# Kernel optimization log

Hardware: AMD Instinct MI355X
Metric: run time of the kernel (lower is better)

## Reference

```python
import jax, jax.numpy as jnp
import numpy as np

N1 = 64
N2 = 64
K = 12        # k_max truncated Fourier modes
L = 4         # num_layers
CIN = 1
COUT = 1
B, H, W = 16, 256, 256


def _conv1x1(x, w, b):
    # x: [B,Ci,H,W], w: [Co,Ci], b: [Co]
    return jnp.einsum('bchw,oc->bohw', x, w) + b[None, :, None, None]


def _spectral_conv(x, w1, w2):
    # x: [B,C,H,W] real; w1,w2: [Ci,Co,K,K] complex64
    Bb, C, Hh, Ww = x.shape
    x_ft = jnp.fft.rfft2(x, axes=(-2, -1))  # [B,C,H,W//2+1] complex
    top = jnp.einsum('bimn,iomn->bomn', x_ft[:, :, :K, :K], w1)
    bot = jnp.einsum('bimn,iomn->bomn', x_ft[:, :, -K:, :K], w2)
    out_ft = jnp.zeros((Bb, N2, Hh, Ww // 2 + 1), dtype=jnp.complex64)
    out_ft = out_ft.at[:, :, :K, :K].set(top)
    out_ft = out_ft.at[:, :, -K:, :K].set(bot)
    return jnp.fft.irfft2(out_ft, s=(Hh, Ww), axes=(-2, -1))


def setup_inputs() -> dict:
    key = jax.random.key(0)
    ks = jax.random.split(key, 12)
    scale = 1.0 / (N1 * N2)
    inp = {
        'x': jax.random.normal(ks[0], (B, CIN, H, W), jnp.float32),
        'lift_w': jax.random.normal(ks[1], (N1, CIN), jnp.float32) * 0.5,
        'lift_b': jnp.zeros((N1,), jnp.float32),
        'spec1_re': jax.random.normal(ks[2], (L, N1, N2, K, K), jnp.float32) * scale,
        'spec1_im': jax.random.normal(ks[3], (L, N1, N2, K, K), jnp.float32) * scale,
        'spec2_re': jax.random.normal(ks[4], (L, N1, N2, K, K), jnp.float32) * scale,
        'spec2_im': jax.random.normal(ks[5], (L, N1, N2, K, K), jnp.float32) * scale,
        'skip_w': jax.random.normal(ks[6], (L, N2, N1), jnp.float32) * (1.0 / np.sqrt(N1)),
        'skip_b': jnp.zeros((L, N2), jnp.float32),
        'proj_w': jax.random.normal(ks[7], (COUT, N2), jnp.float32) * (1.0 / np.sqrt(N2)),
        'proj_b': jnp.zeros((COUT,), jnp.float32),
    }
    return inp


def reference(x, lift_w, lift_b, spec1_re, spec1_im, spec2_re, spec2_im,
              skip_w, skip_b, proj_w, proj_b):
    h = _conv1x1(x, lift_w, lift_b)  # [B,N1,H,W]
    for l in range(L):
        w1 = (spec1_re[l] + 1j * spec1_im[l]).astype(jnp.complex64)
        w2 = (spec2_re[l] + 1j * spec2_im[l]).astype(jnp.complex64)
        spec = _spectral_conv(h, w1, w2)
        skip = _conv1x1(h, skip_w[l], skip_b[l])
        h = jax.nn.gelu(spec + skip, approximate=False)  # torch nn.GELU default = exact erf
    return _conv1x1(h, proj_w, proj_b)  # [B,Cout,H,W]
```

## Files before the change

### kernel.cpp

```cpp
#include <hip/hip_runtime.h>
#include <math.h>

#define PI2 6.283185307179586f

typedef short  bf16x8 __attribute__((ext_vector_type(8)));
typedef float  f32x4  __attribute__((ext_vector_type(4)));
typedef unsigned int u32x4 __attribute__((ext_vector_type(4)));
typedef unsigned int u32x2 __attribute__((ext_vector_type(2)));

__device__ __forceinline__ float gelu_exact(float x) {
    return 0.5f * x * (1.0f + erff(x * 0.70710678118654752f));
}
__device__ __forceinline__ float gelu_fast(float x) {
    float ax = __builtin_fabsf(x);
    float s  = ax * 0.70710678118654752f;
    float t  = 1.0f / fmaf(0.3275911f, s, 1.0f);
    float u  = fmaf(t, 1.061405429f, -1.453152027f);
    u = fmaf(t, u, 1.421413741f);
    u = fmaf(t, u, -0.284496736f);
    u = fmaf(t, u, 0.254829592f);
    float p  = t * u;
    float e  = __expf(-s * s);
    float q  = 0.5f * ax;
    return fmaf(-q * p, e, fmaf(0.5f, x, q));
}
__device__ __forceinline__ float bf2f(unsigned short u) {
    return __uint_as_float(((unsigned int)u) << 16);
}
__device__ __forceinline__ unsigned short f2bf(float f) {
    unsigned int b = __float_as_uint(f);
    unsigned int r = (b + 0x7FFFu + ((b >> 16) & 1u)) >> 16;
    return (unsigned short)r;
}
__device__ __forceinline__ unsigned cvtpk_bf16(float lo, float hi) {
    unsigned r;
    asm("v_cvt_pk_bf16_f32 %0, %1, %2" : "=v"(r) : "v"(lo), "v"(hi));
    return r;
}
__device__ __forceinline__ unsigned pack_lo(unsigned a, unsigned b) {
    return (a & 0xffffu) | (b << 16);
}
__device__ __forceinline__ unsigned pack_hi(unsigned a, unsigned b) {
    return (a >> 16) | (b & 0xffff0000u);
}

template<bool BF> struct HS;
template<> struct HS<false> {
    using ST = float;
    static __device__ __forceinline__ float4 ld4(const ST* p, size_t i4) {
        return reinterpret_cast<const float4*>(p)[i4];
    }
    static __device__ __forceinline__ void st4(ST* p, size_t i4, float4 v) {
        reinterpret_cast<float4*>(p)[i4] = v;
    }
};
template<> struct HS<true> {
    using ST = unsigned short;
    static __device__ __forceinline__ float4 ld4(const ST* p, size_t i4) {
        ushort4 u = reinterpret_cast<const ushort4*>(p)[i4];
        return make_float4(bf2f(u.x), bf2f(u.y), bf2f(u.z), bf2f(u.w));
    }
    static __device__ __forceinline__ void st4(ST* p, size_t i4, float4 v) {
        ushort4 u = make_ushort4(f2bf(v.x), f2bf(v.y), f2bf(v.z), f2bf(v.w));
        reinterpret_cast<ushort4*>(p)[i4] = u;
    }
};


template<bool BF>
__global__ void k_lift(const float* __restrict__ x, const float* __restrict__ lw,
                       const float* __restrict__ lb, typename HS<BF>::ST* __restrict__ h) {
    int i = blockIdx.x * 256 + threadIdx.x;
    int p4 = i & 16383;
    int bc = i >> 14;
    int c = bc & 63, b = bc >> 6;
    float4 xv = reinterpret_cast<const float4*>(x)[(size_t)b * 16384 + p4];
    float w = lw[c], bias = lb[c];
    float4 o;
    o.x = fmaf(xv.x, w, bias); o.y = fmaf(xv.y, w, bias);
    o.z = fmaf(xv.z, w, bias); o.w = fmaf(xv.w, w, bias);
    HS<BF>::st4(h, i, o);
}

template<bool BF>
__global__ __launch_bounds__(256) void k_coldft(const typename HS<BF>::ST* __restrict__ h,
                                                float2* __restrict__ Xw) {
    using ST = typename HS<BF>::ST;
    __shared__ __align__(16) ST xs[64 * 264];
    __shared__ __align__(16) float2 ct[12 * 258];
    int tid = threadIdx.x;
    size_t row0 = (size_t)blockIdx.x * 64;
#pragma unroll
    for (int k = 0; k < 12; k++) {
        int idx = tid + k * 256;
        int n = idx >> 8, w = idx & 255;
        int rr = (n * w) & 255;
        float s, c;
        __sincosf(PI2 * (float)rr * (1.0f / 256.0f), &s, &c);
        ct[n * 258 + w] = make_float2(c, -s);
    }
    const ST* src = h + row0 * 256;
    if constexpr (BF) {
#pragma unroll
        for (int k = 0; k < 8; k++) {
            int i = (tid + k * 256) * 8;
            int r = i >> 8, w = i & 255;
            uint4 v = *reinterpret_cast<const uint4*>(src + i);
            *reinterpret_cast<uint4*>(&xs[r * 264 + w]) = v;
        }
    } else {
#pragma unroll
        for (int k = 0; k < 16; k++) {
            int i = (tid + k * 256) * 4;
            int r = i >> 8, w = i & 255;
            float4 v = *reinterpret_cast<const float4*>(src + i);
            *reinterpret_cast<float4*>(&xs[r * 264 + w]) = v;
        }
    }
    __syncthreads();
    int r = tid >> 2, g = tid & 3;
    int n0 = g * 3;
    float a0r = 0.f, a0i = 0.f, a1r = 0.f, a1i = 0.f, a2r = 0.f, a2i = 0.f;
    const ST* xrow = &xs[r * 264];
    const float2* c0 = &ct[(n0 + 0) * 258];
    const float2* c1 = &ct[(n0 + 1) * 258];
    const float2* c2 = &ct[(n0 + 2) * 258];
#pragma unroll 8
    for (int wc = 0; wc < 256; wc += 4) {
        float x0, x1, x2, x3;
        if constexpr (BF) {
            ushort4 u = *reinterpret_cast<const ushort4*>(xrow + wc);
            x0 = bf2f(u.x); x1 = bf2f(u.y); x2 = bf2f(u.z); x3 = bf2f(u.w);
        } else {
            float4 f = *reinterpret_cast<const float4*>(xrow + wc);
            x0 = f.x; x1 = f.y; x2 = f.z; x3 = f.w;
        }
        float4 pa, pb;
        pa = *reinterpret_cast<const float4*>(c0 + wc);
        pb = *reinterpret_cast<const float4*>(c0 + wc + 2);
        a0r = fmaf(x0, pa.x, a0r); a0i = fmaf(x0, pa.y, a0i);
        a0r = fmaf(x1, pa.z, a0r); a0i = fmaf(x1, pa.w, a0i);
        a0r = fmaf(x2, pb.x, a0r); a0i = fmaf(x2, pb.y, a0i);
        a0r = fmaf(x3, pb.z, a0r); a0i = fmaf(x3, pb.w, a0i);
        pa = *reinterpret_cast<const float4*>(c1 + wc);
        pb = *reinterpret_cast<const float4*>(c1 + wc + 2);
        a1r = fmaf(x0, pa.x, a1r); a1i = fmaf(x0, pa.y, a1i);
        a1r = fmaf(x1, pa.z, a1r); a1i = fmaf(x1, pa.w, a1i);
        a1r = fmaf(x2, pb.x, a1r); a1i = fmaf(x2, pb.y, a1i);
        a1r = fmaf(x3, pb.z, a1r); a1i = fmaf(x3, pb.w, a1i);
        pa = *reinterpret_cast<const float4*>(c2 + wc);
        pb = *reinterpret_cast<const float4*>(c2 + wc + 2);
        a2r = fmaf(x0, pa.x, a2r); a2i = fmaf(x0, pa.y, a2i);
        a2r = fmaf(x1, pa.z, a2r); a2i = fmaf(x1, pa.w, a2i);
        a2r = fmaf(x2, pb.x, a2r); a2i = fmaf(x2, pb.y, a2i);
        a2r = fmaf(x3, pb.z, a2r); a2i = fmaf(x3, pb.w, a2i);
    }
    size_t bc = row0 >> 8;
    int hrow = (int)(row0 & 255) + r;
    float2* dst = Xw + (bc * 12) * 256 + hrow;
    dst[(size_t)(n0 + 0) * 256] = make_float2(a0r, a0i);
    dst[(size_t)(n0 + 1) * 256] = make_float2(a1r, a1i);
    dst[(size_t)(n0 + 2) * 256] = make_float2(a2r, a2i);
}

__global__ void k_rowdft(const float2* __restrict__ Xw, float2* __restrict__ F) {
    __shared__ float2 sm[12 * 257];
    int bc = blockIdx.x;
    const float2* src = Xw + (size_t)bc * 3072;
    for (int idx = threadIdx.x; idx < 3072; idx += 256) {
        int n = idx >> 8, hh = idx & 255;
        sm[n * 257 + hh] = src[idx];
    }
    __syncthreads();
    for (int j = threadIdx.x; j < 288; j += 256) {
        int n = j % 12, mm = j / 12;
        int meff = (mm < 12) ? mm : mm - 24;
        float s, c;
        __sincosf(-PI2 * (float)meff * (1.0f / 256.0f), &s, &c);
        float br = c, bi = s;
        float tr = 1.f, ti = 0.f, Fr = 0.f, Fi = 0.f;
        for (int hh = 0; hh < 256; hh++) {
            float2 xv = sm[n * 257 + hh];
            Fr = fmaf(xv.x, tr, Fr); Fr = fmaf(-xv.y, ti, Fr);
            Fi = fmaf(xv.x, ti, Fi); Fi = fmaf(xv.y, tr, Fi);
            float nr = tr * br - ti * bi;
            ti = tr * bi + ti * br;
            tr = nr;
        }
        F[(size_t)bc * 288 + j] = make_float2(Fr, Fi);
    }
}

__global__ void k_specmul(const float2* __restrict__ F,
                          const float* __restrict__ s1r, const float* __restrict__ s1i,
                          const float* __restrict__ s2r, const float* __restrict__ s2i,
                          float2* __restrict__ Y, int l) {
    __shared__ float2 wsh[4096];
    int mm = blockIdx.x / 12, n = blockIdx.x % 12;
    const float* wr; const float* wi; int m;
    if (mm < 12) { wr = s1r; wi = s1i; m = mm; }
    else         { wr = s2r; wi = s2i; m = mm - 12; }
    size_t base = (size_t)l * 589824 + (size_t)m * 12 + n;
    for (int idx = threadIdx.x; idx < 4096; idx += 256) {
        size_t a = base + (size_t)idx * 144;
        wsh[idx] = make_float2(wr[a], wi[a]);
    }
    __syncthreads();
    int o = threadIdx.x & 63, bq = threadIdx.x >> 6;
    for (int it = 0; it < 4; it++) {
        int b = bq * 4 + it;
        float Yr = 0.f, Yi = 0.f;
        const float2* Fb = F + (size_t)b * 64 * 288 + mm * 12 + n;
        for (int c = 0; c < 64; c++) {
            float2 fc = Fb[(size_t)c * 288];
            float2 wv = wsh[c * 64 + o];
            Yr = fmaf(fc.x, wv.x, Yr); Yr = fmaf(-fc.y, wv.y, Yr);
            Yi = fmaf(fc.x, wv.y, Yi); Yi = fmaf(fc.y, wv.x, Yi);
        }
        Y[((size_t)b * 64 + o) * 288 + mm * 12 + n] = make_float2(Yr, Yi);
    }
}

__global__ void k_expand(const float2* __restrict__ Y, float2* __restrict__ G) {
    int t = blockIdx.x * 256 + threadIdx.x;
    int hh = t & 255;
    int rem = t >> 8;
    int n = rem % 12, bo = rem / 12;
    const float2* Yb = Y + (size_t)bo * 288 + n;
    float s, c;
    __sincosf(PI2 * (float)hh * (1.0f / 256.0f), &s, &c);
    float br = c, bi = s;
    float tr = 1.f, ti = 0.f, Gr = 0.f, Gi = 0.f;
#pragma unroll
    for (int mm = 0; mm < 12; mm++) {
        float2 yv = Yb[mm * 12];
        Gr = fmaf(yv.x, tr, Gr); Gr = fmaf(-yv.y, ti, Gr);
        Gi = fmaf(yv.x, ti, Gi); Gi = fmaf(yv.y, tr, Gi);
        float nr = tr * br - ti * bi;
        ti = tr * bi + ti * br;
        tr = nr;
    }
    ti = -ti;
#pragma unroll
    for (int mm = 12; mm < 24; mm++) {
        float2 yv = Yb[mm * 12];
        Gr = fmaf(yv.x, tr, Gr); Gr = fmaf(-yv.y, ti, Gr);
        Gi = fmaf(yv.x, ti, Gi); Gi = fmaf(yv.y, tr, Gi);
        float nr = tr * br - ti * bi;
        ti = tr * bi + ti * br;
        tr = nr;
    }
    float sc = (n == 0 ? 1.0f : 2.0f) * (1.0f / 65536.0f);
    G[t] = make_float2(Gr * sc, Gi * sc);
}

template<bool BF>
__global__ __launch_bounds__(256) void k_update(
        typename HS<BF>::ST* __restrict__ h, const float2* __restrict__ G,
        const float* __restrict__ skw, const float* __restrict__ skb, int l) {
    __shared__ float hin[64 * 64];
    __shared__ float swT[64 * 68];
    __shared__ float2 Gs[64 * 12];
    __shared__ float2 ctab[12 * 64];
    int bx = blockIdx.x;
    int wt = bx & 3, hrow = (bx >> 2) & 255, b = bx >> 10;
    int w0 = wt * 64;
    int tid = threadIdx.x;
    size_t base4 = (size_t)b * 1048576 + (size_t)hrow * 64 + (w0 >> 2);
#pragma unroll
    for (int k = 0; k < 4; k++) {
        int idx = tid + k * 256;
        int c = idx >> 4, q = idx & 15;
        reinterpret_cast<float4*>(hin)[c * 16 + q] =
            HS<BF>::ld4(h, base4 + (size_t)c * 16384 + q);
    }
#pragma unroll
    for (int k = 0; k < 16; k++) {
        int idx = tid + k * 256;
        swT[(idx & 63) * 68 + (idx >> 6)] = skw[l * 4096 + idx];
    }
#pragma unroll
    for (int k = 0; k < 3; k++) {
        int idx = tid + k * 256;
        int o = idx / 12, n = idx % 12;
        Gs[idx] = G[(((size_t)b * 64 + o) * 12 + n) * 256 + hrow];
    }
#pragma unroll
    for (int k = 0; k < 3; k++) {
        int idx = tid + k * 256;
        int n = idx >> 6, wl = idx & 63;
        int r = (n * (w0 + wl)) & 255;
        float s, c;
        __sincosf(PI2 * (float)r * (1.0f / 256.0f), &s, &c);
        ctab[idx] = make_float2(c, s);
    }
    __syncthreads();
    int wq = tid & 15, oq = tid >> 4;
    float acc[4][4];
#pragma unroll
    for (int jo = 0; jo < 4; jo++) {
        float bias = skb[l * 64 + oq * 4 + jo];
#pragma unroll
        for (int jw = 0; jw < 4; jw++) acc[jo][jw] = bias;
    }
#pragma unroll
    for (int n = 0; n < 12; n++) {
        float2 g0 = Gs[(oq * 4 + 0) * 12 + n];
        float2 g1 = Gs[(oq * 4 + 1) * 12 + n];
        float2 g2 = Gs[(oq * 4 + 2) * 12 + n];
        float2 g3 = Gs[(oq * 4 + 3) * 12 + n];
#pragma unroll
        for (int jw = 0; jw < 4; jw++) {
            float2 cs = ctab[n * 64 + wq * 4 + jw];
            acc[0][jw] = fmaf(g0.x, cs.x, acc[0][jw]); acc[0][jw] = fmaf(-g0.y, cs.y, acc[0][jw]);
            acc[1][jw] = fmaf(g1.x, cs.x, acc[1][jw]); acc[1][jw] = fmaf(-g1.y, cs.y, acc[1][jw]);
            acc[2][jw] = fmaf(g2.x, cs.x, acc[2][jw]); acc[2][jw] = fmaf(-g2.y, cs.y, acc[2][jw]);
            acc[3][jw] = fmaf(g3.x, cs.x, acc[3][jw]); acc[3][jw] = fmaf(-g3.y, cs.y, acc[3][jw]);
        }
    }
    const float4* hin4 = reinterpret_cast<const float4*>(hin);
    const float4* swT4 = reinterpret_cast<const float4*>(swT);
#pragma unroll 4
    for (int c = 0; c < 64; c++) {
        float4 hv = hin4[c * 16 + wq];
        float4 wv = swT4[c * 17 + oq];
        acc[0][0] = fmaf(wv.x, hv.x, acc[0][0]); acc[0][1] = fmaf(wv.x, hv.y, acc[0][1]);
        acc[0][2] = fmaf(wv.x, hv.z, acc[0][2]); acc[0][3] = fmaf(wv.x, hv.w, acc[0][3]);
        acc[1][0] = fmaf(wv.y, hv.x, acc[1][0]); acc[1][1] = fmaf(wv.y, hv.y, acc[1][1]);
        acc[1][2] = fmaf(wv.y, hv.z, acc[1][2]); acc[1][3] = fmaf(wv.y, hv.w, acc[1][3]);
        acc[2][0] = fmaf(wv.z, hv.x, acc[2][0]); acc[2][1] = fmaf(wv.z, hv.y, acc[2][1]);
        acc[2][2] = fmaf(wv.z, hv.z, acc[2][2]); acc[2][3] = fmaf(wv.z, hv.w, acc[2][3]);
        acc[3][0] = fmaf(wv.w, hv.x, acc[3][0]); acc[3][1] = fmaf(wv.w, hv.y, acc[3][1]);
        acc[3][2] = fmaf(wv.w, hv.z, acc[3][2]); acc[3][3] = fmaf(wv.w, hv.w, acc[3][3]);
    }
#pragma unroll
    for (int jo = 0; jo < 4; jo++) {
        int o = oq * 4 + jo;
        float4 r;
        r.x = gelu_exact(acc[jo][0]); r.y = gelu_exact(acc[jo][1]);
        r.z = gelu_exact(acc[jo][2]); r.w = gelu_exact(acc[jo][3]);
        HS<BF>::st4(h, base4 + (size_t)o * 16384 + wq, r);
    }
}

template<bool BF>
__global__ void k_proj(const typename HS<BF>::ST* __restrict__ h, const float* __restrict__ pw,
                       const float* __restrict__ pb, float* __restrict__ out) {
    int i = blockIdx.x * 256 + threadIdx.x;
    int b = i >> 14, p4 = i & 16383;
    size_t hb = (size_t)b * 1048576 + p4;
    float4 acc = make_float4(0.f, 0.f, 0.f, 0.f);
#pragma unroll 8
    for (int c = 0; c < 64; c++) {
        float4 hv = HS<BF>::ld4(h, hb + (size_t)c * 16384);
        float wv = pw[c];
        acc.x = fmaf(hv.x, wv, acc.x); acc.y = fmaf(hv.y, wv, acc.y);
        acc.z = fmaf(hv.z, wv, acc.z); acc.w = fmaf(hv.w, wv, acc.w);
    }
    float bias = pb[0];
    acc.x += bias; acc.y += bias; acc.z += bias; acc.w += bias;
    reinterpret_cast<float4*>(out)[i] = acc;
}

#define SKWHI 22528
#define SKWLO 38912
#define TW2US 55296
__global__ __launch_bounds__(256) void k_ttab(unsigned short* __restrict__ Tg,
                                              const float* __restrict__ skw) {
    int idx = blockIdx.x * 256 + threadIdx.x;
    if (idx >= 79872) return;
    if (idx < 16384) {
        int q = idx & 8191;
        int w = q >> 5, b3 = (q >> 3) & 3;
        int k2 = ((b3 ^ (w & 3)) << 3) | (q & 7);
        float v = 0.f;
        if (k2 < 24) {
            int n = k2 >> 1, r = (n * w) & 255;
            float s, c;
            __sincosf(PI2 * (float)r * (1.0f / 256.0f), &s, &c);
            v = (k2 & 1) ? s : c;
        }
        if (idx < 8192) Tg[idx] = f2bf(v);
        else { unsigned short hi = f2bf(v); Tg[idx] = f2bf(v - bf2f(hi)); }
    } else if (idx < 22528) {
        int q = idx - 16384;
        int n2 = q >> 8, t = q & 255;
        int w = (((t >> 3) ^ (n2 & 7)) << 3) | (t & 7);
        int n = n2 >> 1, r = (n * w) & 255;
        float s, c;
        __sincosf(PI2 * (float)r * (1.0f / 256.0f), &s, &c);
        Tg[idx] = f2bf((n2 & 1) ? s : c);
    } else if (idx < 55296) {
        int q = idx - SKWHI;
        int lo = (q >= 16384);
        q &= 16383;
        float w = skw[q];
        unsigned short hi = f2bf(w);
        Tg[idx] = lo ? f2bf(w - bf2f(hi)) : hi;
    } else {
        int j = idx - TW2US;
        int pair = j >> 1, comp = j & 1;
        int mm = pair >> 8, hh = pair & 255;
        int meff = (mm < 12) ? mm : mm - 24;
        int r = (((-(meff * hh)) % 256) + 256) & 255;
        float s, c;
        __sincosf(PI2 * (float)r * (1.0f / 256.0f), &s, &c);
        reinterpret_cast<float*>(Tg + TW2US)[j] = comp ? s : c;
    }
}

__global__ __launch_bounds__(256) void k_xw0(const float* __restrict__ xg,
                                             const float* __restrict__ lw,
                                             const float* __restrict__ lb,
                                             unsigned short* __restrict__ Xwp) {
    __shared__ float xr[256];
    __shared__ float part[24][9];
    __shared__ float xh[24];
    int blk = blockIdx.x;
    int tid = threadIdx.x;
    if (tid < 64)
        reinterpret_cast<float4*>(xr)[tid] =
            reinterpret_cast<const float4*>(xg + (size_t)blk * 256)[tid];
    __syncthreads();
    if (tid < 192) {
        int n2 = tid % 24, seg = tid / 24;
        int n = n2 >> 1, comp = n2 & 1;
        float acc = 0.f;
#pragma unroll 8
        for (int j = 0; j < 32; j++) {
            int w = seg * 32 + j;
            int r = (n * w) & 255;
            float s, c;
            __sincosf(PI2 * (float)r * (1.0f / 256.0f), &s, &c);
            acc = fmaf(xr[w], comp ? -s : c, acc);
        }
        part[n2][seg] = acc;
    }
    __syncthreads();
    if (tid < 24) {
        float a = 0.f;
#pragma unroll
        for (int s = 0; s < 8; s++) a += part[tid][s];
        xh[tid] = a;
    }
    __syncthreads();
    unsigned* dstw = reinterpret_cast<unsigned*>(Xwp + (size_t)blk * 3072);
#pragma unroll
    for (int q = 0; q < 3; q++) {
        int i = tid + q * 256;
        int c = i / 12, n = i % 12;
        float wr = lw[c];
        float re = fmaf(wr, xh[2 * n], (n == 0) ? lb[c] * 256.0f : 0.0f);
        float im = wr * xh[2 * n + 1];
        unsigned short hre = f2bf(re), him = f2bf(im);
        unsigned short lre = f2bf(re - bf2f(hre)), lim = f2bf(im - bf2f(him));
        dstw[i] = (unsigned)hre | ((unsigned)him << 16);
        dstw[768 + i] = (unsigned)lre | ((unsigned)lim << 16);
    }
}

__global__ __launch_bounds__(256) void k_rowdft2t(const unsigned short* __restrict__ Xwp,
                                                  float2* __restrict__ F,
                                                  const float2* __restrict__ tw2) {
    __shared__ float2 sm[12 * 257];
    int bc = blockIdx.x;
    int b = bc >> 6, c = bc & 63;
    for (int idx = threadIdx.x; idx < 3072; idx += 256) {
        int hh = idx / 12, n = idx % 12;
        size_t base = ((size_t)(b * 256 + hh)) * 3072 + c * 24 + n * 2;
        unsigned hi = *reinterpret_cast<const unsigned*>(Xwp + base);
        unsigned lo = *reinterpret_cast<const unsigned*>(Xwp + base + 1536);
        float re = bf2f((unsigned short)(hi & 0xffff)) + bf2f((unsigned short)(lo & 0xffff));
        float im = bf2f((unsigned short)(hi >> 16)) + bf2f((unsigned short)(lo >> 16));
        sm[n * 257 + hh] = make_float2(re, im);
    }
    __syncthreads();
    for (int j = threadIdx.x; j < 288; j += 256) {
        int n = j % 12, mm = j / 12;
        const float2* twp = tw2 + mm * 256;
        const float2* smp = &sm[n * 257];
        float Fr = 0.f, Fi = 0.f;
#pragma unroll 8
        for (int hh = 0; hh < 256; hh++) {
            float2 xv = smp[hh];
            float2 w = twp[hh];
            Fr = fmaf(xv.x, w.x, Fr); Fr = fmaf(-xv.y, w.y, Fr);
            Fi = fmaf(xv.x, w.y, Fi); Fi = fmaf(xv.y, w.x, Fi);
        }
        F[(size_t)bc * 288 + j] = make_float2(Fr, Fi);
    }
}

__global__ __launch_bounds__(1024) void k_specmul2(const float2* __restrict__ F,
                          const float* __restrict__ s1r, const float* __restrict__ s1i,
                          const float* __restrict__ s2r, const float* __restrict__ s2i,
                          float2* __restrict__ Y, int l) {
    __shared__ float2 wsh[4096];
    __shared__ float2 fsh[1024];
    int mm = blockIdx.x / 12, n = blockIdx.x % 12;
    const float* wr; const float* wi; int m;
    if (mm < 12) { wr = s1r; wi = s1i; m = mm; }
    else         { wr = s2r; wi = s2i; m = mm - 12; }
    size_t base = (size_t)l * 589824 + (size_t)m * 12 + n;
    int tid = threadIdx.x;
#pragma unroll
    for (int k = 0; k < 4; k++) {
        int idx = tid + k * 1024;
        size_t a = base + (size_t)idx * 144;
        wsh[idx] = make_float2(wr[a], wi[a]);
    }
    fsh[tid] = F[(size_t)tid * 288 + mm * 12 + n];
    __syncthreads();
    int o = tid & 63, b = tid >> 6;
    const float2* fb = &fsh[b * 64];
    float Yr = 0.f, Yi = 0.f;
#pragma unroll 8
    for (int c = 0; c < 64; c++) {
        float2 fc = fb[c];
        float2 wv = wsh[c * 64 + o];
        Yr = fmaf(fc.x, wv.x, Yr); Yr = fmaf(-fc.y, wv.y, Yr);
        Yi = fmaf(fc.x, wv.y, Yi); Yi = fmaf(fc.y, wv.x, Yi);
    }
    Y[((size_t)(b * 64 + o)) * 288 + mm * 12 + n] = make_float2(Yr, Yi);
}

__global__ __launch_bounds__(256) void k_expand2(const float2* __restrict__ Y,
                                                 unsigned short* __restrict__ Gpk) {
    __shared__ float2 tw[24];
    int blk = blockIdx.x;
    int hh = blk & 255, b = blk >> 8;
    int t = threadIdx.x;
    if (t < 24) {
        int meff = (t < 12) ? t : t - 24;
        int r = (meff * hh) & 255;
        float s, c;
        __sincosf(PI2 * (float)r * (1.0f / 256.0f), &s, &c);
        tw[t] = make_float2(c, s);
    }
    __syncthreads();
    const float2* Yb = Y + (size_t)b * 64 * 288;
    unsigned short* Gb = Gpk + ((size_t)(b * 256 + hh)) * 3072;
#pragma unroll
    for (int q = 0; q < 3; q++) {
        int i = t * 3 + q;
        int o = i / 12, n = i % 12;
        const float2* Yp = Yb + o * 288 + n;
        float Gr = 0.f, Gi = 0.f;
#pragma unroll
        for (int mm = 0; mm < 24; mm++) {
            float2 yv = Yp[mm * 12];
            float2 w = tw[mm];
            Gr = fmaf(yv.x, w.x, Gr); Gr = fmaf(-yv.y, w.y, Gr);
            Gi = fmaf(yv.x, w.y, Gi); Gi = fmaf(yv.y, w.x, Gi);
        }
        float sc = (n == 0 ? 1.0f : 2.0f) * (1.0f / 65536.0f);
        float gr = Gr * sc, gi = -Gi * sc;
        unsigned short hre = f2bf(gr), him = f2bf(gi);
        unsigned short lre = f2bf(gr - bf2f(hre)), lim = f2bf(gi - bf2f(him));
        int off = o * 24 + n * 2;
        *reinterpret_cast<unsigned*>(Gb + off) = (unsigned)hre | ((unsigned)him << 16);
        *reinterpret_cast<unsigned*>(Gb + 1536 + off) = (unsigned)lre | ((unsigned)lim << 16);
    }
}

template<bool FIRST, bool LAST>
__global__ __launch_bounds__(256, 4) void k_fused3(
        unsigned short* hg, const float* __restrict__ xg,
        const float* __restrict__ lw, const float* __restrict__ lb,
        unsigned short* GXw, const float* __restrict__ skb,
        const float* __restrict__ pw, const float* __restrict__ pb,
        float* __restrict__ outg, const unsigned short* __restrict__ Tg, int l) {
    __shared__ __align__(16) unsigned short lds[17152];
    int tid = threadIdx.x, lane = tid & 63, wid = tid >> 6;
    int lr = lane & 15, lg = lane >> 4;
    int bx = blockIdx.x;
    int hrow = bx & 255, b = bx >> 8;

    if constexpr (FIRST) {
        float* xr = reinterpret_cast<float*>(&lds[16384]);
        if (tid < 64)
            reinterpret_cast<float4*>(xr)[tid] =
                reinterpret_cast<const float4*>(xg + (size_t)bx * 256)[tid];
        __syncthreads();
#pragma unroll
        for (int k = 0; k < 4; k++) {
            int pidx = tid + k * 256;
            int cp = pidx >> 5, w0 = (pidx & 31) * 8;
            int c0 = cp * 2;
            float wa = lw[c0], ba = lb[c0];
            float wb = lw[c0 + 1], bb = lb[c0 + 1];
            int sl = (c0 >> 3) & 7, cl = c0 & 7;
#pragma unroll
            for (int j = 0; j < 8; j++) {
                int w = w0 + j;
                float xv = xr[w];
                unsigned h0 = f2bf(fmaf(xv, wa, ba));
                unsigned h1 = f2bf(fmaf(xv, wb, bb));
                int Xws = (w & 7) ^ ((w >> 3) & 7);
                *reinterpret_cast<unsigned*>(&lds[w * 64 + (((sl ^ Xws) & 7) << 3) + cl]) =
                    h0 | (h1 << 16);
            }
        }
    } else {
#pragma unroll
        for (int k = 0; k < 4; k++) {
            int pidx = tid + k * 256;
            int cp = pidx >> 5, w0 = (pidx & 31) * 8;
            int c0 = cp * 2;
            const unsigned short* s0 = hg + ((size_t)(b * 64 + c0) * 256 + hrow) * 256 + w0;
            uint4 v0 = *reinterpret_cast<const uint4*>(s0);
            uint4 v1 = *reinterpret_cast<const uint4*>(s0 + 65536);
            unsigned pr[8];
            pr[0] = pack_lo(v0.x, v1.x); pr[1] = pack_hi(v0.x, v1.x);
            pr[2] = pack_lo(v0.y, v1.y); pr[3] = pack_hi(v0.y, v1.y);
            pr[4] = pack_lo(v0.z, v1.z); pr[5] = pack_hi(v0.z, v1.z);
            pr[6] = pack_lo(v0.w, v1.w); pr[7] = pack_hi(v0.w, v1.w);
            int sl = (c0 >> 3) & 7, cl = c0 & 7;
#pragma unroll
            for (int j = 0; j < 8; j++) {
                int w = w0 + j;
                int Xws = (w & 7) ^ ((w >> 3) & 7);
                *reinterpret_cast<unsigned*>(&lds[w * 64 + (((sl ^ Xws) & 7) << 3) + cl]) = pr[j];
            }
        }
    }
    int oA = wid * 16 + lr;
    bf16x8 bs_h[2], bs_l[2];
#pragma unroll
    for (int ks = 0; ks < 2; ks++) {
        int off = l * 4096 + oA * 64 + ks * 32 + lg * 8;
        bs_h[ks] = __builtin_bit_cast(bf16x8,
            *reinterpret_cast<const u32x4*>(Tg + SKWHI + off));
        bs_l[ks] = __builtin_bit_cast(bf16x8,
            *reinterpret_cast<const u32x4*>(Tg + SKWLO + off));
    }
    int lgc = (lg < 3) ? lg : 2;
    size_t gbase = ((size_t)(b * 256 + hrow)) * 3072 + (size_t)oA * 24 + lgc * 8;
    u32x4 ghv = *reinterpret_cast<const u32x4*>(GXw + gbase);
    u32x4 glv = *reinterpret_cast<const u32x4*>(GXw + gbase + 1536);
    if (lg == 3) { ghv = (u32x4){0, 0, 0, 0}; glv = (u32x4){0, 0, 0, 0}; }
    bf16x8 bg_h = __builtin_bit_cast(bf16x8, ghv);
    bf16x8 bg_l = __builtin_bit_cast(bf16x8, glv);
    float bias_o = skb[l * 64 + oA];
    f32x4 binit = {bias_o, bias_o, bias_o, bias_o};

    __syncthreads();

    f32x4 acc[16];
#pragma unroll
    for (int wt = 0; wt < 16; wt++) acc[wt] = binit;
#pragma unroll
    for (int wt = 0; wt < 16; wt++) {
        int w = wt * 16 + lr;
        int Xws = (w & 7) ^ ((w >> 3) & 7);
        int i0 = w * 64 + (((lg ^ Xws) & 7) << 3);
        int i1 = w * 64 + ((((4 + lg) ^ Xws) & 7) << 3);
        int it = w * 32 + (((lg ^ (w & 3)) & 3) << 3);
        bf16x8 A0 = __builtin_bit_cast(bf16x8, *reinterpret_cast<const u32x4*>(&lds[i0]));
        bf16x8 A1 = __builtin_bit_cast(bf16x8, *reinterpret_cast<const u32x4*>(&lds[i1]));
        bf16x8 Th = __builtin_bit_cast(bf16x8, *reinterpret_cast<const u32x4*>(Tg + it));
        bf16x8 Tl = __builtin_bit_cast(bf16x8, *reinterpret_cast<const u32x4*>(Tg + 8192 + it));
        acc[wt] = __builtin_amdgcn_mfma_f32_16x16x32_bf16(A0, bs_h[0], acc[wt], 0, 0, 0);
        acc[wt] = __builtin_amdgcn_mfma_f32_16x16x32_bf16(A0, bs_l[0], acc[wt], 0, 0, 0);
        acc[wt] = __builtin_amdgcn_mfma_f32_16x16x32_bf16(A1, bs_h[1], acc[wt], 0, 0, 0);
        acc[wt] = __builtin_amdgcn_mfma_f32_16x16x32_bf16(A1, bs_l[1], acc[wt], 0, 0, 0);
        acc[wt] = __builtin_amdgcn_mfma_f32_16x16x32_bf16(Th, bg_h, acc[wt], 0, 0, 0);
        acc[wt] = __builtin_amdgcn_mfma_f32_16x16x32_bf16(Tl, bg_h, acc[wt], 0, 0, 0);
        acc[wt] = __builtin_amdgcn_mfma_f32_16x16x32_bf16(Th, bg_l, acc[wt], 0, 0, 0);
    }
    __syncthreads();

    int wD = lg * 4;
#pragma unroll
    for (int wt = 0; wt < 16; wt++) {
        float v0 = gelu_fast(acc[wt][0]);
        float v1 = gelu_fast(acc[wt][1]);
        float v2 = gelu_fast(acc[wt][2]);
        float v3 = gelu_fast(acc[wt][3]);
        u32x2 pk;
        pk[0] = cvtpk_bf16(v0, v1);
        pk[1] = cvtpk_bf16(v2, v3);
        *reinterpret_cast<u32x2*>(&lds[oA * 268 + wt * 16 + wD]) = pk;
    }
    __syncthreads();

    if constexpr (LAST) {
        float accp = pb[0];
#pragma unroll 8
        for (int o = 0; o < 64; o++)
            accp = fmaf(pw[o], bf2f(lds[o * 268 + tid]), accp);
        outg[(size_t)bx * 256 + tid] = accp;
        return;
    }

#pragma unroll
    for (int k = 0; k < 8; k++) {
        int chi = k * 256 + tid;
        int o = chi >> 5, wq = (chi & 31) * 8;
        u32x2 lo = *reinterpret_cast<const u32x2*>(&lds[o * 268 + wq]);
        u32x2 hi = *reinterpret_cast<const u32x2*>(&lds[o * 268 + wq + 4]);
        uint4 v = make_uint4(lo[0], lo[1], hi[0], hi[1]);
        *reinterpret_cast<uint4*>(hg + ((size_t)(b * 64 + o) * 256 + hrow) * 256 + wq) = v;
    }
    f32x4 acc2[2];
    acc2[0] = (f32x4){0.f, 0.f, 0.f, 0.f};
    acc2[1] = (f32x4){0.f, 0.f, 0.f, 0.f};
    int oa = wid * 16 + lr;
#pragma unroll
    for (int sg = 0; sg < 8; sg++) {
        int wb = 4 * sg + lg;
        u32x2 alo = *reinterpret_cast<const u32x2*>(&lds[oa * 268 + wb * 8]);
        u32x2 ahi = *reinterpret_cast<const u32x2*>(&lds[oa * 268 + wb * 8 + 4]);
        u32x4 av = {alo[0], alo[1], ahi[0], ahi[1]};
        bf16x8 Af = __builtin_bit_cast(bf16x8, av);
#pragma unroll
        for (int nt = 0; nt < 2; nt++) {
            int n2 = nt * 16 + lr;
            int n2r = (n2 < 24) ? n2 : 23;
            bf16x8 Bf = __builtin_bit_cast(bf16x8, *reinterpret_cast<const u32x4*>(
                Tg + 16384 + n2r * 256 + ((wb ^ (n2r & 7)) << 3)));
            acc2[nt] = __builtin_amdgcn_mfma_f32_16x16x32_bf16(Af, Bf, acc2[nt], 0, 0, 0);
        }
    }
    __syncthreads();
    int oD = wid * 16 + lg * 4;
#pragma unroll
    for (int nt = 0; nt < 2; nt++) {
        int n2 = nt * 16 + lr;
        if (n2 < 24) {
            float sgn = (n2 & 1) ? -1.f : 1.f;
#pragma unroll
            for (int r = 0; r < 4; r++) {
                float v = sgn * acc2[nt][r];
                unsigned short hv = f2bf(v);
                unsigned short lv = f2bf(v - bf2f(hv));
                int o = oD + r;
                lds[o * 24 + n2] = hv;
                lds[1536 + o * 24 + n2] = lv;
            }
        }
    }
    __syncthreads();
    unsigned* dstw = reinterpret_cast<unsigned*>(GXw + ((size_t)(b * 256 + hrow)) * 3072);
    const unsigned* srcw = reinterpret_cast<const unsigned*>(lds);
#pragma unroll
    for (int q = 0; q < 3; q++) {
        int i = tid + q * 256;
        dstw[i] = srcw[i];
    }
}


template<bool BF>
static void run_pipeline_old(void* const* d_in, void* d_out, void* d_ws, hipStream_t stream) {
    const float* x   = (const float*)d_in[0];
    const float* lw  = (const float*)d_in[1];
    const float* lb  = (const float*)d_in[2];
    const float* s1r = (const float*)d_in[3];
    const float* s1i = (const float*)d_in[4];
    const float* s2r = (const float*)d_in[5];
    const float* s2i = (const float*)d_in[6];
    const float* skw = (const float*)d_in[7];
    const float* skb = (const float*)d_in[8];
    const float* pw  = (const float*)d_in[9];
    const float* pb  = (const float*)d_in[10];
    float* out = (float*)d_out;
    char* ws = (char*)d_ws;
    using ST = typename HS<BF>::ST;
    size_t hbytes = 67108864ull * sizeof(ST);
    ST*     hbuf = (ST*)ws;
    float2* XwG  = (float2*)(ws + hbytes);
    float2* F    = (float2*)(ws + hbytes + 25165824ull);
    float2* Y    = (float2*)(ws + hbytes + 25165824ull + 2359296ull);
    k_lift<BF><<<65536, 256, 0, stream>>>(x, lw, lb, hbuf);
    for (int l = 0; l < 4; l++) {
        k_coldft<BF><<<4096, 256, 0, stream>>>(hbuf, XwG);
        k_rowdft <<<1024,  256, 0, stream>>>(XwG, F);
        k_specmul<<<288,   256, 0, stream>>>(F, s1r, s1i, s2r, s2i, Y, l);
        k_expand <<<12288, 256, 0, stream>>>(Y, XwG);
        k_update<BF><<<16384, 256, 0, stream>>>(hbuf, XwG, skw, skb, l);
    }
    k_proj<BF><<<1024, 256, 0, stream>>>(hbuf, pw, pb, out);
}

static void run_pipeline_fused(void* const* d_in, void* d_out, void* d_ws, hipStream_t stream) {
    const float* x   = (const float*)d_in[0];
    const float* lw  = (const float*)d_in[1];
    const float* lb  = (const float*)d_in[2];
    const float* s1r = (const float*)d_in[3];
    const float* s1i = (const float*)d_in[4];
    const float* s2r = (const float*)d_in[5];
    const float* s2i = (const float*)d_in[6];
    const float* skw = (const float*)d_in[7];
    const float* skb = (const float*)d_in[8];
    const float* pw  = (const float*)d_in[9];
    const float* pb  = (const float*)d_in[10];
    float* out = (float*)d_out;
    char* ws = (char*)d_ws;
    unsigned short* hbuf = (unsigned short*)ws;
    unsigned short* XwG  = (unsigned short*)(ws + 134217728ull);
    float2* F   = (float2*)(ws + 134217728ull + 25165824ull);
    float2* Y   = (float2*)(ws + 134217728ull + 25165824ull + 2359296ull);
    unsigned short* Tg = (unsigned short*)(ws + 164102144ull);
    const float2* tw2 = (const float2*)((char*)Tg + 110592);

    k_ttab<<<312, 256, 0, stream>>>(Tg, skw);
    k_xw0<<<4096, 256, 0, stream>>>(x, lw, lb, XwG);
    for (int l = 0; l < 4; l++) {
        k_rowdft2t<<<1024, 256, 0, stream>>>(XwG, F, tw2);
        k_specmul2<<<288, 1024, 0, stream>>>(F, s1r, s1i, s2r, s2i, Y, l);
        k_expand2<<<4096, 256, 0, stream>>>(Y, XwG);
        if (l == 0)
            k_fused3<true, false><<<4096, 256, 0, stream>>>(hbuf, x, lw, lb, XwG, skb, pw, pb, out, Tg, l);
        else if (l == 3)
            k_fused3<false, true><<<4096, 256, 0, stream>>>(hbuf, x, lw, lb, XwG, skb, pw, pb, out, Tg, l);
        else
            k_fused3<false, false><<<4096, 256, 0, stream>>>(hbuf, x, lw, lb, XwG, skb, pw, pb, out, Tg, l);
    }
}

extern "C" void kernel_launch(void* const* d_in, const int* in_sizes, int n_in,
                              void* d_out, int out_size, void* d_ws, size_t ws_size,
                              hipStream_t stream) {
    if (ws_size >= 164261888ull) {
        run_pipeline_fused(d_in, d_out, d_ws, stream);
    } else {
        run_pipeline_old<true>(d_in, d_out, d_ws, stream);
    }
}
```

Before: 818.5 us.

## Shrink fused-layer LDS with XOR swizzle, raise occupancy, streamline lift and packing

The padded 268-stride LDS layout is replaced by a 256-stride XOR-swizzled layout, which shrinks shared memory to 32 KB. That allows launch bounds of 5 blocks per CU and turns the split 8-byte LDS reads into single 16-byte reads. The first layer now loads its x values straight from global memory instead of staging them through LDS, which removes a barrier, and it uses the hardware packed bf16 convert. Channel packing uses v_perm_b32. The higher occupancy target may force register spills.

```diff
diff --git a/kernel.cpp b/kernel.cpp
--- a/kernel.cpp
+++ b/kernel.cpp
@@ -35,6 +35,16 @@
 __device__ __forceinline__ unsigned cvtpk_bf16(float lo, float hi) {
     unsigned r;
     asm("v_cvt_pk_bf16_f32 %0, %1, %2" : "=v"(r) : "v"(lo), "v"(hi));
+    return r;
+}
+__device__ __forceinline__ unsigned perm_lo(unsigned a, unsigned b) {
+    unsigned r;
+    asm("v_perm_b32 %0, %1, %2, %3" : "=v"(r) : "v"(b), "v"(a), "s"(0x05040100u));
+    return r;
+}
+__device__ __forceinline__ unsigned perm_hi(unsigned a, unsigned b) {
+    unsigned r;
+    asm("v_perm_b32 %0, %1, %2, %3" : "=v"(r) : "v"(b), "v"(a), "s"(0x07060302u));
     return r;
 }
 __device__ __forceinline__ unsigned pack_lo(unsigned a, unsigned b) {
@@ -564,24 +574,19 @@
 }
 
 template<bool FIRST, bool LAST>
-__global__ __launch_bounds__(256, 4) void k_fused3(
+__global__ __launch_bounds__(256, 5) void k_fused3(
         unsigned short* hg, const float* __restrict__ xg,
         const float* __restrict__ lw, const float* __restrict__ lb,
         unsigned short* GXw, const float* __restrict__ skb,
         const float* __restrict__ pw, const float* __restrict__ pb,
         float* __restrict__ outg, const unsigned short* __restrict__ Tg, int l) {
-    __shared__ __align__(16) unsigned short lds[17152];
+    __shared__ __align__(16) unsigned short lds[16384];
     int tid = threadIdx.x, lane = tid & 63, wid = tid >> 6;
     int lr = lane & 15, lg = lane >> 4;
     int bx = blockIdx.x;
     int hrow = bx & 255, b = bx >> 8;
 
     if constexpr (FIRST) {
-        float* xr = reinterpret_cast<float*>(&lds[16384]);
-        if (tid < 64)
-            reinterpret_cast<float4*>(xr)[tid] =
-                reinterpret_cast<const float4*>(xg + (size_t)bx * 256)[tid];
-        __syncthreads();
 #pragma unroll
         for (int k = 0; k < 4; k++) {
             int pidx = tid + k * 256;
@@ -589,16 +594,18 @@
             int c0 = cp * 2;
             float wa = lw[c0], ba = lb[c0];
             float wb = lw[c0 + 1], bb = lb[c0 + 1];
+            float4 xv0 = *reinterpret_cast<const float4*>(xg + (size_t)bx * 256 + w0);
+            float4 xv1 = *reinterpret_cast<const float4*>(xg + (size_t)bx * 256 + w0 + 4);
+            float xv[8] = {xv0.x, xv0.y, xv0.z, xv0.w, xv1.x, xv1.y, xv1.z, xv1.w};
             int sl = (c0 >> 3) & 7, cl = c0 & 7;
 #pragma unroll
             for (int j = 0; j < 8; j++) {
                 int w = w0 + j;
-                float xv = xr[w];
-                unsigned h0 = f2bf(fmaf(xv, wa, ba));
-                unsigned h1 = f2bf(fmaf(xv, wb, bb));
+                float h0 = fmaf(xv[j], wa, ba);
+                float h1 = fmaf(xv[j], wb, bb);
                 int Xws = (w & 7) ^ ((w >> 3) & 7);
                 *reinterpret_cast<unsigned*>(&lds[w * 64 + (((sl ^ Xws) & 7) << 3) + cl]) =
-                    h0 | (h1 << 16);
+                    cvtpk_bf16(h0, h1);
             }
         }
     } else {
@@ -611,10 +618,10 @@
             uint4 v0 = *reinterpret_cast<const uint4*>(s0);
             uint4 v1 = *reinterpret_cast<const uint4*>(s0 + 65536);
             unsigned pr[8];
-            pr[0] = pack_lo(v0.x, v1.x); pr[1] = pack_hi(v0.x, v1.x);
-            pr[2] = pack_lo(v0.y, v1.y); pr[3] = pack_hi(v0.y, v1.y);
-            pr[4] = pack_lo(v0.z, v1.z); pr[5] = pack_hi(v0.z, v1.z);
-            pr[6] = pack_lo(v0.w, v1.w); pr[7] = pack_hi(v0.w, v1.w);
+            pr[0] = perm_lo(v0.x, v1.x); pr[1] = perm_hi(v0.x, v1.x);
+            pr[2] = perm_lo(v0.y, v1.y); pr[3] = perm_hi(v0.y, v1.y);
+            pr[4] = perm_lo(v0.z, v1.z); pr[5] = perm_hi(v0.z, v1.z);
+            pr[6] = perm_lo(v0.w, v1.w); pr[7] = perm_hi(v0.w, v1.w);
             int sl = (c0 >> 3) & 7, cl = c0 & 7;
 #pragma unroll
             for (int j = 0; j < 8; j++) {
@@ -671,6 +678,7 @@
     __syncthreads();
 
     int wD = lg * 4;
+    int osw = (oA & 7) << 3;
 #pragma unroll
     for (int wt = 0; wt < 16; wt++) {
         float v0 = gelu_fast(acc[wt][0]);
@@ -680,7 +688,7 @@
         u32x2 pk;
         pk[0] = cvtpk_bf16(v0, v1);
         pk[1] = cvtpk_bf16(v2, v3);
-        *reinterpret_cast<u32x2*>(&lds[oA * 268 + wt * 16 + wD]) = pk;
+        *reinterpret_cast<u32x2*>(&lds[oA * 256 + ((wt * 16 + wD) ^ osw)]) = pk;
     }
     __syncthreads();
 
@@ -688,7 +696,7 @@
         float accp = pb[0];
 #pragma unroll 8
         for (int o = 0; o < 64; o++)
-            accp = fmaf(pw[o], bf2f(lds[o * 268 + tid]), accp);
+            accp = fmaf(pw[o], bf2f(lds[o * 256 + (tid ^ ((o & 7) << 3))]), accp);
         outg[(size_t)bx * 256 + tid] = accp;
         return;
     }
@@ -697,22 +705,19 @@
     for (int k = 0; k < 8; k++) {
         int chi = k * 256 + tid;
         int o = chi >> 5, wq = (chi & 31) * 8;
-        u32x2 lo = *reinterpret_cast<const u32x2*>(&lds[o * 268 + wq]);
-        u32x2 hi = *reinterpret_cast<const u32x2*>(&lds[o * 268 + wq + 4]);
-        uint4 v = make_uint4(lo[0], lo[1], hi[0], hi[1]);
-        *reinterpret_cast<uint4*>(hg + ((size_t)(b * 64 + o) * 256 + hrow) * 256 + wq) = v;
+        u32x4 v = *reinterpret_cast<const u32x4*>(&lds[o * 256 + (wq ^ ((o & 7) << 3))]);
+        *reinterpret_cast<u32x4*>(hg + ((size_t)(b * 64 + o) * 256 + hrow) * 256 + wq) = v;
     }
     f32x4 acc2[2];
     acc2[0] = (f32x4){0.f, 0.f, 0.f, 0.f};
     acc2[1] = (f32x4){0.f, 0.f, 0.f, 0.f};
     int oa = wid * 16 + lr;
+    int oasw = (oa & 7) << 3;
 #pragma unroll
     for (int sg = 0; sg < 8; sg++) {
         int wb = 4 * sg + lg;
-        u32x2 alo = *reinterpret_cast<const u32x2*>(&lds[oa * 268 + wb * 8]);
-        u32x2 ahi = *reinterpret_cast<const u32x2*>(&lds[oa * 268 + wb * 8 + 4]);
-        u32x4 av = {alo[0], alo[1], ahi[0], ahi[1]};
-        bf16x8 Af = __builtin_bit_cast(bf16x8, av);
+        bf16x8 Af = __builtin_bit_cast(bf16x8,
+            *reinterpret_cast<const u32x4*>(&lds[oa * 256 + ((wb * 8) ^ oasw)]));
 #pragma unroll
         for (int nt = 0; nt < 2; nt++) {
             int n2 = nt * 16 + lr;
```

New measurement: 936.7 us. 14.4% more time.
